# Kernel tuning notes

Measured on AMD Instinct MI355X. Metric: run time of the kernel, lower is better.

Reference implementation:

```python
import jax, jax.numpy as jnp
import numpy as np

T, B, D, H = 512, 128, 1024, 1024


def setup_inputs() -> dict:
    key = jax.random.key(0)
    ks = jax.random.split(key, 6)
    obs = jax.random.normal(ks[0], (T, B, D), jnp.float32)
    resets = jax.random.randint(ks[1], (T, B), 0, 2).astype(bool)
    h0 = jax.random.normal(ks[2], (B, H), jnp.float32)
    c0 = jax.random.normal(ks[3], (B, H), jnp.float32)
    s_in = 1.0 / np.sqrt(D)
    s_h = 1.0 / np.sqrt(H)
    # Fused gate weights in flax order (i, f, g, o) along the last axis.
    Wx = jax.random.uniform(ks[4], (D, 4 * H), jnp.float32, -s_in, s_in)
    Wh = jax.random.uniform(ks[5], (H, 4 * H), jnp.float32, -s_h, s_h)
    b = jnp.zeros((4 * H,), jnp.float32)
    return {"obs": obs, "resets": resets, "h0": h0, "c0": c0, "Wx": Wx, "Wh": Wh, "b": b}


def reference(obs, resets, h0, c0, Wx, Wh, b):
    # obs: [T, B, D], resets: [T, B] bool, h0/c0: [B, H]
    def step(carry, xs):
        h, c = carry
        x, r = xs
        m = r[:, None]
        # initialize_carry returns zeros -> reset masking zeroes the state
        h = jnp.where(m, jnp.zeros_like(h), h)
        c = jnp.where(m, jnp.zeros_like(c), c)
        gates = x @ Wx + h @ Wh + b  # [B, 4H]
        i, f, g, o = jnp.split(gates, 4, axis=-1)
        new_c = jax.nn.sigmoid(f) * c + jax.nn.sigmoid(i) * jnp.tanh(g)
        new_h = jax.nn.sigmoid(o) * jnp.tanh(new_c)
        return (new_h, new_c), new_h

    (hT, cT), out = jax.lax.scan(step, (h0, c0), (obs, resets))
    return out, hT, cT
```

## Files before the change

### kernel.cpp

```cpp
#include <hip/hip_runtime.h>
#include <hip/hip_bf16.h>

#define TT 512
#define BB 128
#define DD 1024
#define HH 1024
#define NG 4096
#define KT 2048

using bf8    = __attribute__((ext_vector_type(8))) short;
using f32x4  = __attribute__((ext_vector_type(4))) float;
using f32x16 = __attribute__((ext_vector_type(16))) float;

__device__ __forceinline__ unsigned short f2bf(float f) {
  unsigned int u = __builtin_bit_cast(unsigned int, f);
  u += 0x7fffu + ((u >> 16) & 1u);
  return (unsigned short)(u >> 16);
}
__device__ __forceinline__ float bf2f(unsigned short u) {
  unsigned int x = ((unsigned int)u) << 16;
  return __builtin_bit_cast(float, x);
}
__device__ __forceinline__ float sigm(float x) { return 1.0f / (1.0f + __expf(-x)); }
__device__ __forceinline__ float ftanh(float x) {
  float e = __expf(2.0f * x);
  return 1.0f - 2.0f / (e + 1.0f);
}


__global__ void k_detect(const unsigned int* __restrict__ rw, int* __restrict__ flagmode,
                         unsigned int* __restrict__ flags) {
  __shared__ int any;
  if (threadIdx.x == 0) any = 0;
  __syncthreads();
  int loc = 0;
  for (int i = threadIdx.x; i < (TT * BB) / 4; i += blockDim.x)
    if (rw[i] > 1u) loc = 1;
  if (loc) atomicOr(&any, 1);
  __syncthreads();
  if (threadIdx.x == 0) *flagmode = any;
  flags[threadIdx.x] = 1u;
}

__global__ void k_pack(const float* __restrict__ Wx, const float* __restrict__ Wh,
                       unsigned short* __restrict__ Wp) {
  __shared__ unsigned short tile[64][65];
  const int kt = blockIdx.x & 31;
  const int nt = blockIdx.x >> 5;
  const int k0 = kt * 64, n0 = nt * 64;
  const int t = threadIdx.x;
  {
    const int kl = t >> 2;
    const int nl = (t & 3) * 16;
    const int kg = k0 + kl;
    const float* src = (kg < DD) ? (Wx + (size_t)kg * NG + n0 + nl)
                                 : (Wh + (size_t)(kg - DD) * NG + n0 + nl);
#pragma unroll
    for (int j = 0; j < 16; ++j) tile[kl][nl + j] = f2bf(src[j]);
  }
  __syncthreads();
  {
    const int nl = t >> 2;
    const int kl = (t & 3) * 16;
    unsigned short* dst = Wp + (size_t)(n0 + nl) * KT + k0 + kl;
#pragma unroll
    for (int j = 0; j < 16; ++j) dst[j] = tile[kl + j][nl];
  }
}

__global__ void k_initB3(const float* __restrict__ h0, const unsigned char* __restrict__ rB,
                         const int* __restrict__ rI, const int* __restrict__ flagmode,
                         unsigned short* __restrict__ hbufB) {
  const int i = blockIdx.x * 256 + threadIdx.x;
  if (i >= BB * HH) return;
  const int row = i >> 10, hcol = i & 1023;
  const bool r = (*flagmode) ? (rB[row] != 0) : (rI[row] != 0);
  const unsigned short val = r ? (unsigned short)0 : f2bf(h0[i]);
  const int g = row >> 5, rl = row & 31;
  const size_t e = (size_t)g * 32768 + (size_t)(hcol >> 4) * 512
                 + (size_t)((hcol >> 3) & 1) * 256 + (size_t)rl * 8 + (hcol & 7);
  hbufB[e] = val;
}

__global__ void k_cvt(const float* __restrict__ src, unsigned short* __restrict__ dst) {
  size_t i = ((size_t)blockIdx.x * 256 + threadIdx.x) * 8;
  const size_t stride = (size_t)2048 * 256 * 8;
  for (; i < (size_t)TT * BB * DD; i += stride) {
    f32x4 a = *(const f32x4*)(src + i);
    f32x4 c = *(const f32x4*)(src + i + 4);
    uint4 cv;
    asm("v_cvt_pk_bf16_f32 %0, %1, %2" : "=v"(cv.x) : "v"(a[0]), "v"(a[1]));
    asm("v_cvt_pk_bf16_f32 %0, %1, %2" : "=v"(cv.y) : "v"(a[2]), "v"(a[3]));
    asm("v_cvt_pk_bf16_f32 %0, %1, %2" : "=v"(cv.z) : "v"(c[0]), "v"(c[1]));
    asm("v_cvt_pk_bf16_f32 %0, %1, %2" : "=v"(cv.w) : "v"(c[2]), "v"(c[3]));
    *(bf8*)(dst + i) = __builtin_bit_cast(bf8, cv);
  }
}

#define GEMM_SMEM 69632

__global__ void __launch_bounds__(256)
k_gemm(const unsigned short* __restrict__ A, const unsigned short* __restrict__ Bw,
       unsigned short* __restrict__ C) {
  extern __shared__ char gsm[];
  const int tid = threadIdx.x;
  const int w = tid >> 6, l = tid & 63;
  const int l15 = l & 15, lh4 = l >> 4;
  const int wm2 = w >> 1, wn2 = w & 1;
  const int bid0 = blockIdx.x;
  const int swz = (bid0 & 7) * 2048 + (bid0 >> 3);
  const int mt = swz >> 5, nt = swz & 31;
  const size_t m0 = (size_t)mt * 128, n0 = (size_t)nt * 128;

  f32x4 acc[4][4] = {};

  const int srow = l >> 3;
  const int schunk = (l & 7) ^ srow;

  const unsigned short* Ag[4];
  const unsigned short* Bg[4];
#pragma unroll
  for (int i = 0; i < 4; ++i) {
    const int r = w * 32 + i * 8 + srow;
    Ag[i] = A + (m0 + r) * 1024 + schunk * 8;
    Bg[i] = Bw + (n0 + r) * 2048 + schunk * 8;
  }

#define GSTAGE(BUF, KS) do {                                                        \
    const size_t ko_ = (size_t)(KS) * 64;                                           \
    char* base_ = gsm + (BUF) * 32768;                                              \
    _Pragma("unroll")                                                               \
    for (int i_ = 0; i_ < 4; ++i_) {                                                \
      __builtin_amdgcn_global_load_lds(                                             \
        (const __attribute__((address_space(1))) unsigned int*)(Ag[i_] + ko_),      \
        (__attribute__((address_space(3))) unsigned int*)(base_ + (w*32 + i_*8)*128), \
        16, 0, 0);                                                                  \
      __builtin_amdgcn_global_load_lds(                                             \
        (const __attribute__((address_space(1))) unsigned int*)(Bg[i_] + ko_),      \
        (__attribute__((address_space(3))) unsigned int*)(base_ + 16384 + (w*32 + i_*8)*128), \
        16, 0, 0);                                                                  \
    }                                                                               \
  } while (0)

#define GCOMP(BUF) do {                                                             \
    const char* bA_ = gsm + (BUF) * 32768;                                          \
    const char* bB_ = bA_ + 16384;                                                  \
    _Pragma("unroll")                                                               \
    for (int kk_ = 0; kk_ < 2; ++kk_) {                                             \
      bf8 af_[4], bf_[4];                                                           \
      _Pragma("unroll")                                                             \
      for (int mi_ = 0; mi_ < 4; ++mi_) {                                           \
        const int r_ = wm2 * 64 + mi_ * 16 + l15;                                   \
        af_[mi_] = *(const bf8*)(bA_ + r_ * 128 + ((kk_*64 + lh4*16) ^ ((r_ & 7) << 4))); \
      }                                                                             \
      _Pragma("unroll")                                                             \
      for (int ni_ = 0; ni_ < 4; ++ni_) {                                           \
        const int r_ = wn2 * 64 + ni_ * 16 + l15;                                   \
        bf_[ni_] = *(const bf8*)(bB_ + r_ * 128 + ((kk_*64 + lh4*16) ^ ((r_ & 7) << 4))); \
      }                                                                             \
      _Pragma("unroll")                                                             \
      for (int mi_ = 0; mi_ < 4; ++mi_)                                             \
        _Pragma("unroll")                                                           \
        for (int ni_ = 0; ni_ < 4; ++ni_)                                           \
          acc[mi_][ni_] = __builtin_amdgcn_mfma_f32_16x16x32_bf16(                  \
              af_[mi_], bf_[ni_], acc[mi_][ni_], 0, 0, 0);                          \
    }                                                                               \
  } while (0)

  GSTAGE(0, 0);
  asm volatile("s_waitcnt vmcnt(0)" ::: "memory");
  __syncthreads();
#pragma unroll 1
  for (int ks = 0; ks < 16; ++ks) {
    if (ks < 15) GSTAGE((ks + 1) & 1, ks + 1);
    GCOMP(ks & 1);
    if (ks < 15) {
      asm volatile("s_waitcnt vmcnt(0)" ::: "memory");
      __syncthreads();
    }
  }

  __syncthreads();
  float* ct = (float*)(gsm + w * 17408);
#pragma unroll
  for (int mi = 0; mi < 4; ++mi)
#pragma unroll
    for (int ni = 0; ni < 4; ++ni)
#pragma unroll
      for (int q = 0; q < 4; ++q)
        ct[(mi * 16 + lh4 * 4 + q) * 68 + ni * 16 + l15] = acc[mi][ni][q];
#pragma unroll
  for (int i = 0; i < 8; ++i) {
    const int row = i * 8 + (l >> 3);
    const int c8 = (l & 7) * 8;
    f32x4 v0 = *(const f32x4*)(ct + row * 68 + c8);
    f32x4 v1 = *(const f32x4*)(ct + row * 68 + c8 + 4);
    uint4 cv;
    asm("v_cvt_pk_bf16_f32 %0, %1, %2" : "=v"(cv.x) : "v"(v0[0]), "v"(v0[1]));
    asm("v_cvt_pk_bf16_f32 %0, %1, %2" : "=v"(cv.y) : "v"(v0[2]), "v"(v0[3]));
    asm("v_cvt_pk_bf16_f32 %0, %1, %2" : "=v"(cv.z) : "v"(v1[0]), "v"(v1[1]));
    asm("v_cvt_pk_bf16_f32 %0, %1, %2" : "=v"(cv.w) : "v"(v1[2]), "v"(v1[3]));
    *(bf8*)(C + (m0 + wm2 * 64 + row) * 4096 + n0 + wn2 * 64 + c8) =
        __builtin_bit_cast(bf8, cv);
  }
#undef GSTAGE
#undef GCOMP
}

#define SCANH3_SMEM 155648
#define TMP3_OFF 131072
#define HSLOT3 262144

#define HI3(I) asm volatile("global_load_dwordx4 %0, %1, off sc0 sc1" \
    : "=v"(ha[I]) : "v"(hbB + (I) * 1024) : "memory")

#define BRD3(CI, CN) (*(const bf8*)(sm + \
    (size_t)((((CI) * 2 + lhi) * 64 + (CN) * 32 + l31)) * 16))

#define HC3(CI, VM) do {                                                  \
    bf8 nb0, nb1;                                                         \
    if ((CI) < 15) { nb0 = BRD3(kc0 + (CI) + 1, 0); nb1 = BRD3(kc0 + (CI) + 1, 1); } \
    asm volatile("s_waitcnt vmcnt(" #VM ")" ::: "memory");                \
    __builtin_amdgcn_sched_barrier(0);                                    \
    ac0 = __builtin_amdgcn_mfma_f32_32x32x16_bf16(ha[CI], cb0, ac0, 0, 0, 0); \
    ac1 = __builtin_amdgcn_mfma_f32_32x32x16_bf16(ha[CI], cb1, ac1, 0, 0, 0); \
    cb0 = nb0; cb1 = nb1;                                                 \
  } while (0)

__global__ void __launch_bounds__(256)
k_scanh3(const unsigned char* __restrict__ resetsB, const int* __restrict__ resetsI,
         const float* __restrict__ c0, const float* __restrict__ bias,
         const unsigned short* __restrict__ Wp, const unsigned short* __restrict__ gx,
         unsigned short* __restrict__ hbufB, unsigned int* __restrict__ flags,
         const int* __restrict__ flagmode, float* __restrict__ out) {
  extern __shared__ char sm[];
  float* TG = (float*)(sm + TMP3_OFF);

  const int tid = threadIdx.x;
  const int wq  = tid >> 6;
  const int ln  = tid & 63;
  const int l31 = ln & 31;
  const int lhi = ln >> 5;
  const int kc0 = wq * 16;
  const int bid = blockIdx.x;
  const int g   = bid >> 6;
  const int b   = bid & 63;
  const int byteMode = *flagmode;

  {
    const int c = tid >> 2, seg = tid & 3;
    const int n = (c >> 4) * 1024 + b * 16 + (c & 15);
    const unsigned short* src = Wp + (size_t)n * KT + 1024;
#pragma unroll 8
    for (int i = 0; i < 32; ++i) {
      const int k8 = seg * 32 + i;
      bf8 v = *(const bf8*)(src + k8 * 8);
      *(bf8*)(sm + ((size_t)k8 * 64 + c) * 16) = v;
    }
  }

  const int row  = tid >> 3;
  const int jd   = tid & 7;
  const int grow = g * 32 + row;
  const int hc   = b * 16 + jd * 2;

  float ccx = c0[(size_t)grow * HH + hc];
  float ccy = c0[(size_t)grow * HH + hc + 1];
  const float bx0 = bias[0 * HH + hc], by0 = bias[0 * HH + hc + 1];
  const float bx1 = bias[1 * HH + hc], by1 = bias[1 * HH + hc + 1];
  const float bx2 = bias[2 * HH + hc], by2 = bias[2 * HH + hc + 1];
  const float bx3 = bias[3 * HH + hc], by3 = bias[3 * HH + hc + 1];

  const size_t puboff = (size_t)(hc >> 4) * 1024 + (size_t)((hc >> 3) & 1) * 512
                      + (size_t)row * 16 + (size_t)(hc & 7) * 2;

  __syncthreads();

#pragma unroll 1
  for (int t = 0; t < TT; ++t) {
    const unsigned short* gp = gx + ((size_t)t * BB + grow) * 4096 + hc;
    const unsigned int gx0 = *(const unsigned int*)(gp);
    const unsigned int gx1 = *(const unsigned int*)(gp + 1024);
    const unsigned int gx2 = *(const unsigned int*)(gp + 2048);
    const unsigned int gx3 = *(const unsigned int*)(gp + 3072);
    bool rc, rn = false;
    if (byteMode) {
      rc = resetsB[t * BB + grow] != 0;
      if (t + 1 < TT) rn = resetsB[(t + 1) * BB + grow] != 0;
    } else {
      rc = resetsI[t * BB + grow] != 0;
      if (t + 1 < TT) rn = resetsI[(t + 1) * BB + grow] != 0;
    }

    {
      const unsigned int need = (unsigned int)(t + 1);
      const unsigned int* fp = flags + g * 64;
      while (true) {
        unsigned int v = __hip_atomic_load(&fp[ln], __ATOMIC_RELAXED,
                                           __HIP_MEMORY_SCOPE_AGENT);
        if (__all(v >= need)) break;
        __builtin_amdgcn_s_sleep(2);
      }
    }
    asm volatile("" ::: "memory");
    __builtin_amdgcn_sched_barrier(0);

    f32x16 ac0 = {0.f,0.f,0.f,0.f, 0.f,0.f,0.f,0.f, 0.f,0.f,0.f,0.f, 0.f,0.f,0.f,0.f};
    f32x16 ac1 = {0.f,0.f,0.f,0.f, 0.f,0.f,0.f,0.f, 0.f,0.f,0.f,0.f, 0.f,0.f,0.f,0.f};
    {
      const char* hbB = (const char*)hbufB + (size_t)(t & 1) * HSLOT3
                      + (size_t)g * 65536 + (size_t)kc0 * 1024
                      + (size_t)lhi * 512 + (size_t)l31 * 16;
      bf8 ha[16];
      HI3(0);  HI3(1);  HI3(2);  HI3(3);  HI3(4);  HI3(5);  HI3(6);  HI3(7);
      HI3(8);  HI3(9);  HI3(10); HI3(11); HI3(12); HI3(13); HI3(14); HI3(15);
      bf8 cb0 = BRD3(kc0, 0), cb1 = BRD3(kc0, 1);
      HC3(0, 15);  HC3(1, 14);  HC3(2, 13);  HC3(3, 12);
      HC3(4, 11);  HC3(5, 10);  HC3(6, 9);   HC3(7, 8);
      HC3(8, 7);   HC3(9, 6);   HC3(10, 5);  HC3(11, 4);
      HC3(12, 3);  HC3(13, 2);  HC3(14, 1);  HC3(15, 0);
    }

    if (wq > 0) {
      char* tp = sm + TMP3_OFF + (wq - 1) * 8192 + ln * 16;
#pragma unroll
      for (int qd = 0; qd < 4; ++qd) {
        f32x4 v0 = {ac0[qd*4+0], ac0[qd*4+1], ac0[qd*4+2], ac0[qd*4+3]};
        f32x4 v1 = {ac1[qd*4+0], ac1[qd*4+1], ac1[qd*4+2], ac1[qd*4+3]};
        *(f32x4*)(tp + qd * 1024)        = v0;
        *(f32x4*)(tp + 4096 + qd * 1024) = v1;
      }
    }
    __syncthreads();
    if (wq == 0) {
#pragma unroll
      for (int s = 0; s < 3; ++s) {
        const char* tp = sm + TMP3_OFF + s * 8192 + ln * 16;
#pragma unroll
        for (int qd = 0; qd < 4; ++qd) {
          f32x4 v0 = *(const f32x4*)(tp + qd * 1024);
          f32x4 v1 = *(const f32x4*)(tp + 4096 + qd * 1024);
          ac0[qd*4+0] += v0[0]; ac0[qd*4+1] += v0[1];
          ac0[qd*4+2] += v0[2]; ac0[qd*4+3] += v0[3];
          ac1[qd*4+0] += v1[0]; ac1[qd*4+1] += v1[1];
          ac1[qd*4+2] += v1[2]; ac1[qd*4+3] += v1[3];
        }
      }
    }
    __syncthreads();
    if (wq == 0) {
#pragma unroll
      for (int r = 0; r < 16; ++r) {
        const int rowl = (r & 3) + 8 * (r >> 2) + 4 * lhi;
        TG[rowl * 66 + l31]      = ac0[r];
        TG[rowl * 66 + 32 + l31] = ac1[r];
      }
    }
    __syncthreads();

    const float* GLr = TG + row * 66;
    const int hl = jd * 2;
    const float i0 = GLr[ 0 + hl]     + bf2f((unsigned short)(gx0 & 0xffff)) + bx0;
    const float i1 = GLr[ 0 + hl + 1] + bf2f((unsigned short)(gx0 >> 16))    + by0;
    const float f0 = GLr[16 + hl]     + bf2f((unsigned short)(gx1 & 0xffff)) + bx1;
    const float f1 = GLr[16 + hl + 1] + bf2f((unsigned short)(gx1 >> 16))    + by1;
    const float g0 = GLr[32 + hl]     + bf2f((unsigned short)(gx2 & 0xffff)) + bx2;
    const float g1 = GLr[32 + hl + 1] + bf2f((unsigned short)(gx2 >> 16))    + by2;
    const float o0 = GLr[48 + hl]     + bf2f((unsigned short)(gx3 & 0xffff)) + bx3;
    const float o1 = GLr[48 + hl + 1] + bf2f((unsigned short)(gx3 >> 16))    + by3;
    const float cox = rc ? 0.f : ccx;
    const float coy = rc ? 0.f : ccy;
    const float ncx = sigm(f0) * cox + sigm(i0) * ftanh(g0);
    const float ncy = sigm(f1) * coy + sigm(i1) * ftanh(g1);
    const float nhx = sigm(o0) * ftanh(ncx);
    const float nhy = sigm(o1) * ftanh(ncy);
    ccx = ncx; ccy = ncy;

    if (t + 1 < TT) {
      const float hx = rn ? 0.f : nhx, hy = rn ? 0.f : nhy;
      unsigned int hp;
      asm("v_cvt_pk_bf16_f32 %0, %1, %2" : "=v"(hp) : "v"(hx), "v"(hy));
      char* dst = (char*)hbufB + (size_t)((t + 1) & 1) * HSLOT3
                + (size_t)g * 65536 + puboff;
      asm volatile("global_store_dword %0, %1, off sc0 sc1" :: "v"(dst), "v"(hp) : "memory");
      asm volatile("s_waitcnt vmcnt(0)" ::: "memory");
      __syncthreads();
      if (tid == 0) {
        unsigned int* fp = flags + bid;
        const unsigned int val = (unsigned int)(t + 2);
        asm volatile("global_store_dword %0, %1, off sc0 sc1" :: "v"(fp), "v"(val) : "memory");
      }
      float* op = out + (size_t)t * BB * HH + (size_t)grow * HH + hc;
      op[0] = nhx; op[1] = nhy;
    } else {
      float* op = out + (size_t)t * BB * HH + (size_t)grow * HH + hc;
      op[0] = nhx; op[1] = nhy;
      float* hp2 = out + (size_t)TT * BB * HH + (size_t)grow * HH + hc;
      hp2[0] = nhx; hp2[1] = nhy;
      float* cp2 = out + (size_t)TT * BB * HH + (size_t)BB * HH + (size_t)grow * HH + hc;
      cp2[0] = ncx; cp2[1] = ncy;
    }
  }
}


extern "C" void kernel_launch(void* const* d_in, const int* in_sizes, int n_in,
                              void* d_out, int out_size, void* d_ws, size_t ws_size,
                              hipStream_t stream) {
  const float* obs  = (const float*)d_in[0];
  const void*  rst  = d_in[1];
  const float* h0   = (const float*)d_in[2];
  const float* c0   = (const float*)d_in[3];
  const float* Wx   = (const float*)d_in[4];
  const float* Wh   = (const float*)d_in[5];
  const float* bias = (const float*)d_in[6];
  float* out = (float*)d_out;

  char* ws = (char*)d_ws;
  const size_t WP_OFF    = 0;
  const size_t FLAGS_OFF = ((size_t)16 << 20) + ((size_t)512 << 10);
  const size_t HBUFB_OFF = (size_t)17 << 20;
  const size_t OBSBF_OFF = (size_t)24 << 20;
  const size_t GX_OFF    = OBSBF_OFF + ((size_t)128 << 20);

  unsigned short* Wp    = (unsigned short*)(ws + WP_OFF);
  unsigned int*   flags = (unsigned int*)(ws + FLAGS_OFF);
  int*        flagmode  = (int*)(flags + 1024);
  unsigned short* hbufB = (unsigned short*)(ws + HBUFB_OFF);
  unsigned short* obsbf = (unsigned short*)(ws + OBSBF_OFF);
  unsigned short* gxp   = (unsigned short*)(ws + GX_OFF);

  const unsigned char* rB = (const unsigned char*)rst;
  const int* rI = (const int*)rst;

  k_detect<<<1, 256, 0, stream>>>((const unsigned int*)rst, flagmode, flags);
  k_pack<<<dim3((KT / 64) * (NG / 64)), dim3(256), 0, stream>>>(Wx, Wh, Wp);
  k_initB3<<<dim3((BB * HH) / 256), dim3(256), 0, stream>>>(h0, rB, rI, flagmode, hbufB);
  k_cvt<<<dim3(2048), dim3(256), 0, stream>>>(obs, obsbf);
  hipFuncSetAttribute((const void*)k_gemm,
                      hipFuncAttributeMaxDynamicSharedMemorySize, GEMM_SMEM);
  k_gemm<<<dim3((TT * BB / 128) * (NG / 128)), dim3(256), GEMM_SMEM, stream>>>(
      obsbf, Wp, gxp);

  hipFuncSetAttribute((const void*)k_scanh3,
                      hipFuncAttributeMaxDynamicSharedMemorySize, SCANH3_SMEM);
  void* args3[] = { (void*)&rB, (void*)&rI, (void*)&c0, (void*)&bias, (void*)&Wp,
                    (void*)&gxp, (void*)&hbufB, (void*)&flags, (void*)&flagmode,
                    (void*)&out };
  hipLaunchCooperativeKernel((const void*)k_scanh3, dim3(256), dim3(256), args3,
                             SCANH3_SMEM, stream);
}
```

Baseline: 2.720 ms.

## Drop GEMM block swizzle, use acquire fence instead of uncached h loads, merge syncs

Several small changes at once. The GEMM block-index swizzle is removed in favour of plain row-major tile order. In the recurrent scan, the hidden-state loads no longer use the sc0 sc1 cache-bypass bits; correctness now relies on an agent-scope acquire fence after the flag spin. One __syncthreads between the partial-sum reduction and the TG store is removed, since only wave 0 does both. Uncached loads are swapped for cached loads plus a fence, which may lower per-step latency but depends on the fence invalidating stale L2 or L1 lines.

Result: slower. 6.267 ms (+130.4%).

```diff
diff --git a/kernel.cpp b/kernel.cpp
--- a/kernel.cpp
+++ b/kernel.cpp
@@ -107,9 +107,7 @@
   const int w = tid >> 6, l = tid & 63;
   const int l15 = l & 15, lh4 = l >> 4;
   const int wm2 = w >> 1, wn2 = w & 1;
-  const int bid0 = blockIdx.x;
-  const int swz = (bid0 & 7) * 2048 + (bid0 >> 3);
-  const int mt = swz >> 5, nt = swz & 31;
+  const int mt = blockIdx.x >> 5, nt = blockIdx.x & 31;
   const size_t m0 = (size_t)mt * 128, n0 = (size_t)nt * 128;
 
   f32x4 acc[4][4] = {};
@@ -207,11 +205,11 @@
 #undef GCOMP
 }
 
-#define SCANH3_SMEM 155648
-#define TMP3_OFF 131072
+#define SCANH_SMEM 155648
+#define TMP_OFF 131072
 #define HSLOT3 262144
 
-#define HI3(I) asm volatile("global_load_dwordx4 %0, %1, off sc0 sc1" \
+#define HI3(I) asm volatile("global_load_dwordx4 %0, %1, off" \
     : "=v"(ha[I]) : "v"(hbB + (I) * 1024) : "memory")
 
 #define BRD3(CI, CN) (*(const bf8*)(sm + \
@@ -228,13 +226,13 @@
   } while (0)
 
 __global__ void __launch_bounds__(256)
-k_scanh3(const unsigned char* __restrict__ resetsB, const int* __restrict__ resetsI,
-         const float* __restrict__ c0, const float* __restrict__ bias,
-         const unsigned short* __restrict__ Wp, const unsigned short* __restrict__ gx,
-         unsigned short* __restrict__ hbufB, unsigned int* __restrict__ flags,
-         const int* __restrict__ flagmode, float* __restrict__ out) {
+k_scanh(const unsigned char* __restrict__ resetsB, const int* __restrict__ resetsI,
+        const float* __restrict__ c0, const float* __restrict__ bias,
+        const unsigned short* __restrict__ Wp, const unsigned short* __restrict__ gx,
+        unsigned short* __restrict__ hbufB, unsigned int* __restrict__ flags,
+        const int* __restrict__ flagmode, float* __restrict__ out) {
   extern __shared__ char sm[];
-  float* TG = (float*)(sm + TMP3_OFF);
+  float* TG = (float*)(sm + TMP_OFF);
 
   const int tid = threadIdx.x;
   const int wq  = tid >> 6;
@@ -302,7 +300,7 @@
         __builtin_amdgcn_s_sleep(2);
       }
     }
-    asm volatile("" ::: "memory");
+    __builtin_amdgcn_fence(__ATOMIC_ACQUIRE, "agent");
     __builtin_amdgcn_sched_barrier(0);
 
     f32x16 ac0 = {0.f,0.f,0.f,0.f, 0.f,0.f,0.f,0.f, 0.f,0.f,0.f,0.f, 0.f,0.f,0.f,0.f};
@@ -322,7 +320,7 @@
     }
 
     if (wq > 0) {
-      char* tp = sm + TMP3_OFF + (wq - 1) * 8192 + ln * 16;
+      char* tp = sm + TMP_OFF + (wq - 1) * 8192 + ln * 16;
 #pragma unroll
       for (int qd = 0; qd < 4; ++qd) {
         f32x4 v0 = {ac0[qd*4+0], ac0[qd*4+1], ac0[qd*4+2], ac0[qd*4+3]};
@@ -335,7 +333,7 @@
     if (wq == 0) {
 #pragma unroll
       for (int s = 0; s < 3; ++s) {
-        const char* tp = sm + TMP3_OFF + s * 8192 + ln * 16;
+        const char* tp = sm + TMP_OFF + s * 8192 + ln * 16;
 #pragma unroll
         for (int qd = 0; qd < 4; ++qd) {
           f32x4 v0 = *(const f32x4*)(tp + qd * 1024);
@@ -346,9 +344,6 @@
           ac1[qd*4+2] += v1[2]; ac1[qd*4+3] += v1[3];
         }
       }
-    }
-    __syncthreads();
-    if (wq == 0) {
 #pragma unroll
       for (int r = 0; r < 16; ++r) {
         const int rowl = (r & 3) + 8 * (r >> 2) + 4 * lhi;
@@ -442,11 +437,11 @@
   k_gemm<<<dim3((TT * BB / 128) * (NG / 128)), dim3(256), GEMM_SMEM, stream>>>(
       obsbf, Wp, gxp);
 
-  hipFuncSetAttribute((const void*)k_scanh3,
-                      hipFuncAttributeMaxDynamicSharedMemorySize, SCANH3_SMEM);
+  hipFuncSetAttribute((const void*)k_scanh,
+                      hipFuncAttributeMaxDynamicSharedMemorySize, SCANH_SMEM);
   void* args3[] = { (void*)&rB, (void*)&rI, (void*)&c0, (void*)&bias, (void*)&Wp,
                     (void*)&gxp, (void*)&hbufB, (void*)&flags, (void*)&flagmode,
                     (void*)&out };
-  hipLaunchCooperativeKernel((const void*)k_scanh3, dim3(256), dim3(256), args3,
-                             SCANH3_SMEM, stream);
-}
+  hipLaunchCooperativeKernel((const void*)k_scanh, dim3(256), dim3(256), args3,
+                             SCANH_SMEM, stream);
+}
```
